# Kernel optimization log

Measured on AMD Instinct MI355X. Metric: run time of the kernel, lower is better.

## Reference

```python
import jax, jax.numpy as jnp
import numpy as np

ALPHA = 0.2   # LeakyReLU negative slope (init arg alpha)
H = 256       # hidden_dim
U = 1024      # user pairs -> 2U user nodes
M = 64        # UAV nodes
D = 2 * U     # uniform out-degree per UAV (edges sorted by source)
N = 2 * U + M
E = M * D


def _lstm_dir(x, w_ih, w_hh, b):
    # x: [T, B, I] -> outputs [T, B, Hc]; b = b_ih + b_hh (they only ever add)
    Hc = w_hh.shape[1]
    B = x.shape[1]
    def step(carry, xt):
        h, c = carry
        g = xt @ w_ih.T + h @ w_hh.T + b          # [B, 4*Hc], gate order i,f,g,o
        i, f, gg, o = jnp.split(g, 4, axis=-1)
        c = jax.nn.sigmoid(f) * c + jax.nn.sigmoid(i) * jnp.tanh(gg)
        h = jax.nn.sigmoid(o) * jnp.tanh(c)
        return (h, c), h
    h0 = jnp.zeros((B, Hc), x.dtype)
    _, hs = jax.lax.scan(step, (h0, h0), x)
    return hs


def _bilstm(x, wih, whh, b):
    # wih: [2, 4Hc, I]; whh: [2, 4Hc, Hc]; b: [2, 4Hc]; dir 0 = fwd, 1 = reverse
    fwd = _lstm_dir(x, wih[0], whh[0], b[0])
    rev = _lstm_dir(x[::-1], wih[1], whh[1], b[1])[::-1]
    return jnp.concatenate([fwd, rev], axis=-1)   # [T, B, 2*Hc]


def _mlp2(h, w1, b1, w2, b2):
    h = jax.nn.relu(h @ w1.T + b1)
    return jax.nn.relu(h @ w2.T + b2)


def _forward(x, edge_index, users_num,
             ul_wih, ul_whh, ul_b, uav_lin_w, uav_lin_b,
             msg_w1, msg_b1, msg_w2, msg_b2,
             wq_w, wq_b, wr_w, wr_b, att_w, att_b,
             upd_w1, upd_b1, upd_w2, upd_b2,
             uavl_wih, uavl_whh, uavl_b, lin2_w, lin2_b):
    Un = users_num
    n = x.shape[0]
    m = n - 2 * Un
    # ---- users bidirectional LSTM over the pair (seq_len=2, batch=U) ----
    seq = jnp.stack([x[:Un], x[Un:2 * Un]], axis=0)        # [2, U, 2]
    users = _bilstm(seq, ul_wih, ul_whh, ul_b)             # [2, U, H]
    users = jnp.concatenate([users[0], users[1]], axis=0)  # [2U, H]
    uavs = x[2 * Un:] @ uav_lin_w.T + uav_lin_b            # [M, H]
    h = jnp.concatenate([users, uavs], axis=0)             # [N, H]
    # ---- message passing (flow target_to_source: i=src, aggregate at src) ----
    src, tgt = edge_index[0], edge_index[1]
    xi = h[src]                                            # [E, H]
    xj = h[tgt]                                            # [E, H]
    msg = _mlp2(jnp.concatenate([xi, xj], axis=1), msg_w1, msg_b1, msg_w2, msg_b2)  # [E, H]
    q = xi @ wq_w.T + wq_b
    r = msg @ wr_w.T + wr_b
    a = jax.nn.leaky_relu(jnp.concatenate([q, r], axis=1) @ att_w.T + att_b, ALPHA)  # [E,1]
    # segment softmax: edges sorted by source, uniform degree -> reshape [M, D]
    a = jax.nn.softmax(a.reshape(m, -1), axis=1).reshape(-1, 1)
    # ---- scatter-mean aggregate over source index ----
    agg = jax.ops.segment_sum(a * msg, src, num_segments=n)          # [N, H]
    cnt = jax.ops.segment_sum(jnp.ones((src.shape[0],), x.dtype), src, num_segments=n)
    agg = agg / jnp.maximum(cnt, 1.0)[:, None]
    # ---- update ----
    h2 = _mlp2(jnp.concatenate([agg, h], axis=1), upd_w1, upd_b1, upd_w2, upd_b2)  # [N, H]
    uav_seq = h2[2 * Un:][:, None, :]                      # [M, 1, H]
    uav_out = _bilstm(uav_seq, uavl_wih, uavl_whh, uavl_b)[:, 0, :]  # [M, H]
    out = jnp.concatenate([h2[:2 * Un], uav_out], axis=0)
    return jax.nn.sigmoid(out @ lin2_w.T + lin2_b)         # [N, 2]


def setup_inputs():
    key = jax.random.key(0)
    ks = iter(jax.random.split(key, 32))
    p = lambda *s: jax.random.normal(next(ks), s, jnp.float32) * 0.05
    Hc = H // 2
    x = jax.random.uniform(next(ks), (N, 2), jnp.float32)
    src = jnp.repeat(2 * U + jnp.arange(M), D)
    tgt = jnp.tile(jnp.arange(2 * U), M)
    edge_index = jnp.stack([src, tgt]).astype(jnp.int32)
    return dict(
        x=x, edge_index=edge_index, users_num=U,
        ul_wih=p(2, 4 * Hc, 2), ul_whh=p(2, 4 * Hc, Hc), ul_b=p(2, 4 * Hc),
        uav_lin_w=p(H, 2), uav_lin_b=p(H),
        msg_w1=p(H, 2 * H), msg_b1=p(H), msg_w2=p(H, H), msg_b2=p(H),
        wq_w=p(H, H), wq_b=p(H), wr_w=p(H, H), wr_b=p(H),
        att_w=p(1, 2 * H), att_b=p(1),
        upd_w1=p(H, 2 * H), upd_b1=p(H), upd_w2=p(H, H), upd_b2=p(H),
        uavl_wih=p(2, 4 * Hc, H), uavl_whh=p(2, 4 * Hc, Hc), uavl_b=p(2, 4 * Hc),
        lin2_w=p(2, H), lin2_b=p(2),
    )


def reference(x, edge_index, users_num,
              ul_wih, ul_whh, ul_b, uav_lin_w, uav_lin_b,
              msg_w1, msg_b1, msg_w2, msg_b2,
              wq_w, wq_b, wr_w, wr_b, att_w, att_b,
              upd_w1, upd_b1, upd_w2, upd_b2,
              uavl_wih, uavl_whh, uavl_b, lin2_w, lin2_b):
    return _forward(x, edge_index, users_num,
                    ul_wih, ul_whh, ul_b, uav_lin_w, uav_lin_b,
                    msg_w1, msg_b1, msg_w2, msg_b2,
                    wq_w, wq_b, wr_w, wr_b, att_w, att_b,
                    upd_w1, upd_b1, upd_w2, upd_b2,
                    uavl_wih, uavl_whh, uavl_b, lin2_w, lin2_b)
```

## Files before the change

kernel.cpp:

```cpp
#include <hip/hip_runtime.h>
#include <hip/hip_bf16.h>
#include <math.h>

#define UQ   1024
#define NUQ  2048
#define MQ   64
#define NN   2112
#define HD   256

typedef __attribute__((ext_vector_type(4))) float f32x4;
typedef __attribute__((ext_vector_type(8))) __bf16 bf16x8;

#define OFF_HB    0u
#define OFF_HUF   65536u
#define OFF_PUBF  1146880u
#define OFF_PB    2195456u
#define OFF_SPR   2260992u
#define OFF_ATT   2261248u
#define OFF_WHHT  2263552u
#define OFF_WIHT  2787840u
#define OFF_W1F   3836416u
#define OFF_W2F   4098560u
#define OFF_UW1F  4229632u
#define OFF_UW2F  4491776u
#define OFF_CREC  4622848u
#define OFF_H2U   5155328u
#define OFF_PART  5220864u

__device__ __forceinline__ float sigm(float v) { return 1.f / (1.f + expf(-v)); }

__device__ __forceinline__ int huf_idx(int row, int k) {
  return (((row >> 6) * 8 + (k >> 5)) * 4 + ((row >> 4) & 3)) * 512 +
         (((k >> 3) & 3) * 16 + (row & 15)) * 8 + (k & 7);
}
__device__ __forceinline__ int pubf_idx(int row, int k) {
  return (((row >> 8) * 8 + (k >> 5)) * 16 + ((row >> 4) & 15)) * 512 +
         (((k >> 3) & 3) * 16 + (row & 15)) * 8 + (k & 7);
}

__device__ __forceinline__ void gl16(const void* g, void* l) {
  __builtin_amdgcn_global_load_lds((const __attribute__((address_space(1))) void*)g,
                                   (__attribute__((address_space(3))) void*)l, 16, 0, 0);
}

__device__ void tile_transpose_perm(const float* __restrict__ in, int in_ld,
                                    float* __restrict__ out, int out_ld,
                                    int k0, int c0) {
  __shared__ float ldt[64][68];
  const int t = threadIdx.x;
  {
    const int ci = t >> 2, kq = t & 3;
    const int c = c0 + ci;
    const int row = (c & 3) * 128 + (c >> 2);
    const float* src = in + row * in_ld + k0 + kq * 16;
#pragma unroll
    for (int e = 0; e < 4; ++e)
      *(f32x4*)&ldt[ci][kq * 16 + e * 4] = *(const f32x4*)(src + e * 4);
  }
  __syncthreads();
  {
    const int kk = t >> 2, cq = t & 3;
    float* dst = out + (k0 + kk) * out_ld + c0 + cq * 16;
#pragma unroll
    for (int e4 = 0; e4 < 4; ++e4) {
      f32x4 v;
#pragma unroll
      for (int j = 0; j < 4; ++j) v[j] = ldt[cq * 16 + e4 * 4 + j][kk];
      *(f32x4*)(dst + e4 * 4) = v;
    }
  }
}

template<int K>
__device__ void frag_cast16(const float* __restrict__ W, int j0, __bf16* __restrict__ frag) {
  __shared__ float ldc[16][K + 4];
  const int t = threadIdx.x;
  {
    const int jr = t >> 4, kq = t & 15;
    const float* src = W + (j0 + jr) * K + kq * (K / 16);
#pragma unroll
    for (int e = 0; e < K / 64; ++e)
      *(f32x4*)&ldc[jr][kq * (K / 16) + e * 4] = *(const f32x4*)(src + e * 4);
  }
  __syncthreads();
  const int f = j0 >> 4;
  constexpr int nks = K >> 5;
  constexpr int thr_per_ks = 256 / nks;
  constexpr int q_per_thr = 512 / thr_per_ks;
  const int ks = t / thr_per_ks;
  const int q0 = (t % thr_per_ks) * q_per_thr;
#pragma unroll
  for (int h = 0; h < q_per_thr / 8; ++h) {
    bf16x8 v;
#pragma unroll
    for (int e = 0; e < 8; ++e) {
      int q = q0 + h * 8 + e;
      int lane = q >> 3;
      v[e] = (__bf16)ldc[lane & 15][ks * 32 + (lane >> 4) * 8 + (q & 7)];
    }
    *(bf16x8*)(frag + (ks * 16 + f) * 512 + q0 + h * 8) = v;
  }
}

__global__ __launch_bounds__(256) void k0_prep(
    const float* __restrict__ ul_whh, const float* __restrict__ uavl_wih,
    const float* __restrict__ msg_w1, const float* __restrict__ msg_w2,
    const float* __restrict__ upd_w1, const float* __restrict__ upd_w2,
    const float* __restrict__ att_w,  const float* __restrict__ att_b,
    const float* __restrict__ wq_w,   const float* __restrict__ wq_b,
    const float* __restrict__ wr_w,   const float* __restrict__ wr_b,
    char* __restrict__ ws)
{
  const int b = blockIdx.x, t = threadIdx.x;
  if (b < 32) {
    const int dir = b >> 4, tile = b & 15;
    tile_transpose_perm(ul_whh + dir * 65536, 128,
                        (float*)(ws + OFF_WHHT) + dir * 65536, 512,
                        (tile >> 3) * 64, (tile & 7) * 64);
  } else if (b < 96) {
    const int b2 = b - 32, dir = b2 >> 5, tile = b2 & 31;
    tile_transpose_perm(uavl_wih + dir * 131072, 256,
                        (float*)(ws + OFF_WIHT) + dir * 131072, 512,
                        (tile >> 3) * 64, (tile & 7) * 64);
  } else if (b < 112) {
    frag_cast16<256>(msg_w2, (b - 96) * 16, (__bf16*)(ws + OFF_W2F));
  } else if (b < 128) {
    frag_cast16<512>(msg_w1, (b - 112) * 16, (__bf16*)(ws + OFF_W1F));
  } else if (b < 144) {
    frag_cast16<512>(upd_w1, (b - 128) * 16, (__bf16*)(ws + OFF_UW1F));
  } else if (b < 160) {
    frag_cast16<256>(upd_w2, (b - 144) * 16, (__bf16*)(ws + OFF_UW2F));
  } else {
    float* wqa = (float*)(ws + OFF_ATT);
    float* vv  = wqa + 256;
    float* c0  = wqa + 512;
    float sa = 0.f, sr = 0.f;
    for (int j = 0; j < 256; ++j) {
      sa += att_w[j]       * wq_w[j * 256 + t];
      sr += att_w[256 + j] * wr_w[j * 256 + t];
    }
    wqa[t] = sa; vv[t] = sr;
    __shared__ float red[256];
    red[t] = att_w[t] * wq_b[t] + att_w[256 + t] * wr_b[t];
    __syncthreads();
    for (int s = 128; s > 0; s >>= 1) { if (t < s) red[t] += red[t + s]; __syncthreads(); }
    if (t == 0) c0[0] = red[0] + att_b[0];
  }
}

__global__ __launch_bounds__(256) void k1_embed(
    const float* __restrict__ x, const float* __restrict__ ul_wih,
    const float* __restrict__ ul_b, const float* __restrict__ uav_lin_w,
    const float* __restrict__ uav_lin_b, char* __restrict__ ws)
{
  __bf16* huf = (__bf16*)(ws + OFF_HUF);
  const int b = blockIdx.x, tid = threadIdx.x;
  if (b < 256) {
    const float* whhT = (const float*)(ws + OFF_WHHT);
    const int dir = tid >> 7, hc = tid & 127;
    const int u0 = b * 4;
    float wx[4], wy[4], bb[4];
#pragma unroll
    for (int g = 0; g < 4; ++g) {
      int row = g * 128 + hc;
      wx[g] = ul_wih[dir * 1024 + row * 2 + 0];
      wy[g] = ul_wih[dir * 1024 + row * 2 + 1];
      bb[g] = ul_b[dir * 512 + row];
    }
    __shared__ float h1s[2][128][4];
    __shared__ float hout[8][260];
    float c1[4], h1v[4], in1x[4], in1y[4];
#pragma unroll
    for (int uu = 0; uu < 4; ++uu) {
      int u = u0 + uu;
      float ax = x[u * 2], ay = x[u * 2 + 1];
      float bx = x[(UQ + u) * 2], by = x[(UQ + u) * 2 + 1];
      float i0x = dir ? bx : ax, i0y = dir ? by : ay;
      in1x[uu] = dir ? ax : bx; in1y[uu] = dir ? ay : by;
      float gv[4];
#pragma unroll
      for (int g = 0; g < 4; ++g) gv[g] = wx[g] * i0x + wy[g] * i0y + bb[g];
      float ii = sigm(gv[0]), gg = tanhf(gv[2]), oo = sigm(gv[3]);
      c1[uu] = ii * gg;
      h1v[uu] = oo * tanhf(c1[uu]);
      h1s[dir][hc][uu] = h1v[uu];
    }
    __syncthreads();
    float acc[4][4];
#pragma unroll
    for (int uu = 0; uu < 4; ++uu)
#pragma unroll
      for (int g = 0; g < 4; ++g) acc[uu][g] = wx[g] * in1x[uu] + wy[g] * in1y[uu] + bb[g];
    for (int k = 0; k < 128; ++k) {
      f32x4 hv  = *(const f32x4*)&h1s[dir][k][0];
      f32x4 wv4 = *(const f32x4*)(whhT + dir * 65536 + k * 512 + hc * 4);
#pragma unroll
      for (int uu = 0; uu < 4; ++uu)
#pragma unroll
        for (int g = 0; g < 4; ++g) acc[uu][g] += hv[uu] * wv4[g];
    }
    const int col = dir * 128 + hc;
#pragma unroll
    for (int uu = 0; uu < 4; ++uu) {
      float ii = sigm(acc[uu][0]), ff = sigm(acc[uu][1]);
      float gg = tanhf(acc[uu][2]), oo = sigm(acc[uu][3]);
      float c2 = ff * c1[uu] + ii * gg;
      float h2v = oo * tanhf(c2);
      float va = dir ? h2v : h1v[uu];
      float vb = dir ? h1v[uu] : h2v;
      hout[uu][col] = va;
      hout[4 + uu][col] = vb;
    }
    __syncthreads();
    {
      const int lr = tid >> 5, c = tid & 31;
      bf16x8 v;
#pragma unroll
      for (int e = 0; e < 8; ++e) v[e] = (__bf16)hout[lr][c * 8 + e];
      const int node = (lr < 4) ? (u0 + lr) : (UQ + u0 + lr - 4);
      *(bf16x8*)(huf + huf_idx(node, c * 8)) = v;
    }
  } else {
    float* hb = (float*)(ws + OFF_HB);
    const int j = tid;
    const int mb = (b - 256) * 16;
    for (int m = mb; m < mb + 16; ++m) {
      float xa = x[(NUQ + m) * 2], xb = x[(NUQ + m) * 2 + 1];
      float val = xa * uav_lin_w[j * 2] + xb * uav_lin_w[j * 2 + 1] + uav_lin_b[j];
      hb[m * 256 + j] = val;
      huf[huf_idx(NUQ + m, j)] = (__bf16)val;
    }
  }
}

template<int G, int NKS>
__device__ __forceinline__ void frag_gemm_acc_g(const __bf16* __restrict__ Abase, int g0,
                                                const __bf16* __restrict__ Bbase,
                                                f32x4 acc[G][4]) {
  const int lane = threadIdx.x & 63;
  const int cg = threadIdx.x >> 6;
  for (int ks = 0; ks < NKS; ++ks) {
    bf16x8 Af[G], Bf[4];
#pragma unroll
    for (int g = 0; g < G; ++g)
      Af[g] = *(const bf16x8*)(Abase + ((ks * 4 + g0 + g) * 64 + lane) * 8);
#pragma unroll
    for (int f = 0; f < 4; ++f)
      Bf[f] = *(const bf16x8*)(Bbase + ((ks * 16 + cg * 4 + f) * 64 + lane) * 8);
#pragma unroll
    for (int g = 0; g < G; ++g)
#pragma unroll
      for (int f = 0; f < 4; ++f)
        acc[g][f] = __builtin_amdgcn_mfma_f32_16x16x32_bf16(Af[g], Bf[f], acc[g][f], 0, 0, 0);
  }
}

__global__ __launch_bounds__(256) void k2_proj(const float* __restrict__ msg_b1,
                                               char* __restrict__ ws)
{
  const __bf16* huf = (const __bf16*)(ws + OFF_HUF);
  const __bf16* w1f = (const __bf16*)(ws + OFF_W1F);
  const int b = blockIdx.x;
  const int lane = threadIdx.x & 63, cg = threadIdx.x >> 6;
  const int cl = lane & 15, g16 = lane >> 4;
  if (b < 64) {
    f32x4 acc[2][4] = {};
    frag_gemm_acc_g<2, 8>(huf + (b >> 1) * 16384, (b & 1) * 2, w1f + 65536, acc);
    __bf16* pubf = (__bf16*)(ws + OFF_PUBF);
#pragma unroll
    for (int g = 0; g < 2; ++g)
#pragma unroll
      for (int f = 0; f < 4; ++f)
#pragma unroll
        for (int r = 0; r < 4; ++r) {
          int row = b * 32 + g * 16 + g16 * 4 + r;
          int col = cg * 64 + f * 16 + cl;
          pubf[pubf_idx(row, col)] = (__bf16)acc[g][f][r];
        }
  } else if (b == 64) {
    f32x4 acc[4][4] = {};
    frag_gemm_acc_g<4, 8>(huf + 32 * 16384, 0, w1f, acc);
    float* pb = (float*)(ws + OFF_PB);
#pragma unroll
    for (int g = 0; g < 4; ++g)
#pragma unroll
      for (int f = 0; f < 4; ++f)
#pragma unroll
        for (int r = 0; r < 4; ++r) {
          int row = g * 16 + g16 * 4 + r;
          int col = cg * 64 + f * 16 + cl;
          pb[row * 256 + col] = acc[g][f][r] + msg_b1[col];
        }
  } else {
    const float* hb  = (const float*)(ws + OFF_HB);
    const float* wqa = (const float*)(ws + OFF_ATT);
    const float* c0  = wqa + 512;
    float* spr = (float*)(ws + OFF_SPR);
    const int t = threadIdx.x;
    if (t < 64) {
      float s = 0.f;
      for (int k = 0; k < 256; ++k) s += hb[t * 256 + k] * wqa[k];
      spr[t] = s + c0[0];
    }
  }
}

__global__ __launch_bounds__(1024, 2) void k3_edge(const float* __restrict__ msg_b2,
                                                   char* __restrict__ ws)
{
  const char*  PUBF = (const char*)(ws + OFF_PUBF);
  const float* PB   = (const float*)(ws + OFF_PB);
  const float* spr  = (const float*)(ws + OFF_SPR);
  const float* vv   = (const float*)(ws + OFF_ATT) + 256;
  const char*  W2F  = (const char*)(ws + OFF_W2F);
  float* crec = (float*)(ws + OFF_CREC);

  __shared__ __align__(16) char bufA[2][16384];
  __shared__ __align__(16) char bufB[2][16384];
  __shared__ float plds[16][64];
  __shared__ float redmax[16], wds[16];
  __shared__ float wvs[4][256];

  const int m = blockIdx.x >> 3, ch = blockIdx.x & 7;
  const int tid = threadIdx.x, wave = tid >> 6, lane = tid & 63;
  const int cl = lane & 15, g16 = lane >> 4;
  const int rg = wave >> 2, cg = wave & 3;
  const int rot = (m + ch) & 7;
  const float sm = spr[m];
  const char* Asrc = PUBF + ch * 131072;
  const float* pbm = PB + m * 256;

  {
    bf16x8 araw = *(const bf16x8*)(Asrc + rot * 16384 + wave * 1024 + lane * 16);
    gl16(W2F + rot * 16384 + wave * 1024 + lane * 16, &bufB[0][wave * 1024]);
    const float* pbp = pbm + rot * 32 + (lane >> 4) * 8;
    f32x4 p0 = *(const f32x4*)pbp, p1 = *(const f32x4*)(pbp + 4);
    bf16x8 a;
#pragma unroll
    for (int r = 0; r < 4; ++r) {
      a[r]     = (__bf16)fmaxf((float)araw[r]     + p0[r], 0.f);
      a[4 + r] = (__bf16)fmaxf((float)araw[4 + r] + p1[r], 0.f);
    }
    *(bf16x8*)(&bufA[0][wave * 1024 + lane * 16]) = a;
  }
  __syncthreads();

  f32x4 acc[4][4] = {};
  for (int i = 0; i < 8; ++i) {
    const int cur = i & 1;
    bf16x8 arn{};
    f32x4 pn0{}, pn1{};
    if (i < 7) {
      const int ksn = (i + 1 + rot) & 7;
      arn = *(const bf16x8*)(Asrc + ksn * 16384 + wave * 1024 + lane * 16);
      gl16(W2F + ksn * 16384 + wave * 1024 + lane * 16, &bufB[cur ^ 1][wave * 1024]);
      const float* pbp = pbm + ksn * 32 + (lane >> 4) * 8;
      pn0 = *(const f32x4*)pbp;
      pn1 = *(const f32x4*)(pbp + 4);
    }
    bf16x8 Af[4], Bf[4];
#pragma unroll
    for (int g = 0; g < 4; ++g)
      Af[g] = *(const bf16x8*)(&bufA[cur][((rg * 4 + g) * 64 + lane) * 16]);
#pragma unroll
    for (int f = 0; f < 4; ++f)
      Bf[f] = *(const bf16x8*)(&bufB[cur][((cg * 4 + f) * 64 + lane) * 16]);
    __builtin_amdgcn_s_setprio(1);
#pragma unroll
    for (int g = 0; g < 4; ++g)
#pragma unroll
      for (int f = 0; f < 4; ++f)
        acc[g][f] = __builtin_amdgcn_mfma_f32_16x16x32_bf16(Af[g], Bf[f], acc[g][f], 0, 0, 0);
    __builtin_amdgcn_s_setprio(0);
    if (i < 7) {
      bf16x8 a;
#pragma unroll
      for (int r = 0; r < 4; ++r) {
        a[r]     = (__bf16)fmaxf((float)arn[r]     + pn0[r], 0.f);
        a[4 + r] = (__bf16)fmaxf((float)arn[4 + r] + pn1[r], 0.f);
      }
      *(bf16x8*)(&bufA[cur ^ 1][wave * 1024 + lane * 16]) = a;
    }
    __syncthreads();
  }

  float p[4][4] = {};
#pragma unroll
  for (int f = 0; f < 4; ++f) {
    const int j = cg * 64 + f * 16 + cl;
    const float b2j = msg_b2[j], vj = vv[j];
#pragma unroll
    for (int g = 0; g < 4; ++g)
#pragma unroll
      for (int r = 0; r < 4; ++r) {
        float mv = fmaxf(acc[g][f][r] + b2j, 0.f);
        acc[g][f][r] = mv;
        p[g][r] += mv * vj;
      }
  }
#pragma unroll
  for (int mask = 1; mask < 16; mask <<= 1)
#pragma unroll
    for (int g = 0; g < 4; ++g)
#pragma unroll
      for (int r = 0; r < 4; ++r) p[g][r] += __shfl_xor(p[g][r], mask);
  if (cl == 0) {
#pragma unroll
    for (int g = 0; g < 4; ++g)
#pragma unroll
      for (int r = 0; r < 4; ++r) plds[wave][g * 16 + g16 * 4 + r] = p[g][r];
  }
  __syncthreads();

  float lr[4][4], wm = -3.4e38f;
#pragma unroll
  for (int g = 0; g < 4; ++g)
#pragma unroll
    for (int r = 0; r < 4; ++r) {
      int row = g * 16 + g16 * 4 + r;
      float l = plds[rg * 4 + 0][row] + plds[rg * 4 + 1][row] +
                plds[rg * 4 + 2][row] + plds[rg * 4 + 3][row] + sm;
      l = l > 0.f ? l : 0.2f * l;
      lr[g][r] = l;
      wm = fmaxf(wm, l);
    }
  wm = fmaxf(wm, __shfl_xor(wm, 16));
  wm = fmaxf(wm, __shfl_xor(wm, 32));
  if (lane == 0) redmax[wave] = wm;
  __syncthreads();
  float Mc = redmax[0];
#pragma unroll
  for (int i = 1; i < 16; ++i) Mc = fmaxf(Mc, redmax[i]);

  float e[4][4], ds = 0.f;
#pragma unroll
  for (int g = 0; g < 4; ++g)
#pragma unroll
    for (int r = 0; r < 4; ++r) { e[g][r] = __expf(lr[g][r] - Mc); ds += e[g][r]; }
  ds += __shfl_xor(ds, 16);
  ds += __shfl_xor(ds, 32);
  if (lane == 0) wds[wave] = ds;

#pragma unroll
  for (int f = 0; f < 4; ++f) {
    float w = 0.f;
#pragma unroll
    for (int g = 0; g < 4; ++g)
#pragma unroll
      for (int r = 0; r < 4; ++r) w += e[g][r] * acc[g][f][r];
    w += __shfl_xor(w, 16);
    w += __shfl_xor(w, 32);
    if (g16 == 0) wvs[rg][cg * 64 + f * 16 + cl] = w;
  }
  __syncthreads();

  float* rec = crec + (m * 8 + ch) * 260;
  if (tid < 256) rec[tid] = wvs[0][tid] + wvs[1][tid] + wvs[2][tid] + wvs[3][tid];
  if (tid == 0) rec[256] = Mc;
  if (tid == 1) rec[257] = wds[0] + wds[4] + wds[8] + wds[12];
}

__global__ __launch_bounds__(256) void k56_update(
    const float* __restrict__ upd_b1, const float* __restrict__ upd_b2,
    const float* __restrict__ lin2_w, const float* __restrict__ lin2_b,
    float* __restrict__ out, char* __restrict__ ws)
{
  const __bf16* huf  = (const __bf16*)(ws + OFF_HUF);
  const __bf16* uw1f = (const __bf16*)(ws + OFF_UW1F);
  const __bf16* uw2f = (const __bf16*)(ws + OFF_UW2F);

  __shared__ __align__(16) __bf16 l1f[8 * 2 * 512];
  __shared__ __align__(16) __bf16 aggf[8 * 2 * 512];
  __shared__ float scs[32][8];
  __shared__ float sS[32];
  __shared__ float l2p[4][32][2];

  const int b = blockIdx.x, tid = threadIdx.x;
  const int lane = tid & 63, cg = tid >> 6;
  const int cl = lane & 15, g16 = lane >> 4;

  f32x4 acc[2][4] = {};
  if (b < 64) {
    frag_gemm_acc_g<2, 8>(huf + (b >> 1) * 16384, (b & 1) * 2, uw1f + 8 * 16 * 512, acc);
  } else {
    const int m0 = (b - 64) * 32;
    const float* crec = (const float*)(ws + OFF_CREC);
    if (tid < 32) {
      const int m = m0 + tid;
      float mx = -3.4e38f;
      for (int c = 0; c < 8; ++c) mx = fmaxf(mx, crec[(m * 8 + c) * 260 + 256]);
      float S = 0.f;
      for (int c = 0; c < 8; ++c) {
        float sc = __expf(crec[(m * 8 + c) * 260 + 256] - mx);
        scs[tid][c] = sc;
        S += sc * crec[(m * 8 + c) * 260 + 257];
      }
      sS[tid] = S;
    }
    __syncthreads();
    for (int ml = 0; ml < 32; ++ml) {
      float A = 0.f;
#pragma unroll
      for (int c = 0; c < 8; ++c) A += scs[ml][c] * crec[((m0 + ml) * 8 + c) * 260 + tid];
      float agg = A / sS[ml] * (1.f / 2048.f);
      aggf[((tid >> 5) * 2 + (ml >> 4)) * 512 + (((tid >> 3) & 3) * 16 + (ml & 15)) * 8 + (tid & 7)] =
          (__bf16)agg;
    }
    __syncthreads();
    const int g0 = (b - 64) * 2;
    const __bf16* hufu = huf + 32 * 16384;
    for (int ks = 0; ks < 8; ++ks) {
      bf16x8 Af[2], Bf[4];
#pragma unroll
      for (int g = 0; g < 2; ++g)
        Af[g] = *(const bf16x8*)(aggf + ((ks * 2 + g) * 64 + lane) * 8);
#pragma unroll
      for (int f = 0; f < 4; ++f)
        Bf[f] = *(const bf16x8*)(uw1f + ((ks * 16 + cg * 4 + f) * 64 + lane) * 8);
#pragma unroll
      for (int g = 0; g < 2; ++g)
#pragma unroll
        for (int f = 0; f < 4; ++f)
          acc[g][f] = __builtin_amdgcn_mfma_f32_16x16x32_bf16(Af[g], Bf[f], acc[g][f], 0, 0, 0);
    }
    for (int ks = 8; ks < 16; ++ks) {
      bf16x8 Af[2], Bf[4];
#pragma unroll
      for (int g = 0; g < 2; ++g)
        Af[g] = *(const bf16x8*)(hufu + (((ks - 8) * 4 + g0 + g) * 64 + lane) * 8);
#pragma unroll
      for (int f = 0; f < 4; ++f)
        Bf[f] = *(const bf16x8*)(uw1f + ((ks * 16 + cg * 4 + f) * 64 + lane) * 8);
#pragma unroll
      for (int g = 0; g < 2; ++g)
#pragma unroll
        for (int f = 0; f < 4; ++f)
          acc[g][f] = __builtin_amdgcn_mfma_f32_16x16x32_bf16(Af[g], Bf[f], acc[g][f], 0, 0, 0);
    }
  }

#pragma unroll
  for (int g = 0; g < 2; ++g)
#pragma unroll
    for (int f = 0; f < 4; ++f) {
      const int col = cg * 64 + f * 16 + cl;
      const float b1 = upd_b1[col];
#pragma unroll
      for (int r = 0; r < 4; ++r) {
        float v = fmaxf(acc[g][f][r] + b1, 0.f);
        l1f[((col >> 5) * 2 + g) * 512 + (((col >> 3) & 3) * 16 + g16 * 4 + r) * 8 + (col & 7)] =
            (__bf16)v;
      }
    }
  __syncthreads();

  f32x4 a2[2][4] = {};
  for (int ks = 0; ks < 8; ++ks) {
    bf16x8 Af[2], Bf[4];
#pragma unroll
    for (int g = 0; g < 2; ++g)
      Af[g] = *(const bf16x8*)(l1f + ((ks * 2 + g) * 64 + lane) * 8);
#pragma unroll
    for (int f = 0; f < 4; ++f)
      Bf[f] = *(const bf16x8*)(uw2f + ((ks * 16 + cg * 4 + f) * 64 + lane) * 8);
#pragma unroll
    for (int g = 0; g < 2; ++g)
#pragma unroll
      for (int f = 0; f < 4; ++f)
        a2[g][f] = __builtin_amdgcn_mfma_f32_16x16x32_bf16(Af[g], Bf[f], a2[g][f], 0, 0, 0);
  }

  if (b < 64) {
    float d0[2][4] = {}, d1[2][4] = {};
#pragma unroll
    for (int f = 0; f < 4; ++f) {
      const int col = cg * 64 + f * 16 + cl;
      const float b2 = upd_b2[col];
      const float w0 = lin2_w[col], w1 = lin2_w[256 + col];
#pragma unroll
      for (int g = 0; g < 2; ++g)
#pragma unroll
        for (int r = 0; r < 4; ++r) {
          float hv = fmaxf(a2[g][f][r] + b2, 0.f);
          d0[g][r] += hv * w0;
          d1[g][r] += hv * w1;
        }
    }
#pragma unroll
    for (int mask = 1; mask < 16; mask <<= 1)
#pragma unroll
      for (int g = 0; g < 2; ++g)
#pragma unroll
        for (int r = 0; r < 4; ++r) {
          d0[g][r] += __shfl_xor(d0[g][r], mask);
          d1[g][r] += __shfl_xor(d1[g][r], mask);
        }
    if (cl == 0) {
#pragma unroll
      for (int g = 0; g < 2; ++g)
#pragma unroll
        for (int r = 0; r < 4; ++r) {
          l2p[cg][g * 16 + g16 * 4 + r][0] = d0[g][r];
          l2p[cg][g * 16 + g16 * 4 + r][1] = d1[g][r];
        }
    }
    __syncthreads();
    if (tid < 32) {
      float s0 = l2p[0][tid][0] + l2p[1][tid][0] + l2p[2][tid][0] + l2p[3][tid][0] + lin2_b[0];
      float s1 = l2p[0][tid][1] + l2p[1][tid][1] + l2p[2][tid][1] + l2p[3][tid][1] + lin2_b[1];
      const int row = b * 32 + tid;
      out[row * 2 + 0] = 1.f / (1.f + expf(-s0));
      out[row * 2 + 1] = 1.f / (1.f + expf(-s1));
    }
  } else {
    float* h2u = (float*)(ws + OFF_H2U);
    const int m0 = (b - 64) * 32;
#pragma unroll
    for (int g = 0; g < 2; ++g)
#pragma unroll
      for (int f = 0; f < 4; ++f) {
        const int col = cg * 64 + f * 16 + cl;
        const float b2 = upd_b2[col];
#pragma unroll
        for (int r = 0; r < 4; ++r) {
          const int rl = g * 16 + g16 * 4 + r;
          h2u[(m0 + rl) * 256 + col] = fmaxf(a2[g][f][r] + b2, 0.f);
        }
      }
  }
}

__global__ __launch_bounds__(256) void k7a_gates(char* __restrict__ ws)
{
  const float* h2u  = (const float*)(ws + OFF_H2U);
  const float* wihT = (const float*)(ws + OFF_WIHT);
  float* part = (float*)(ws + OFF_PART);
  const int m = blockIdx.x >> 2, kq = blockIdx.x & 3;
  const int tid = threadIdx.x;
  const int dir = tid >> 7, hc = tid & 127;
  __shared__ float xs[64];
  if (tid < 64) xs[tid] = h2u[m * 256 + kq * 64 + tid];
  __syncthreads();
  f32x4 a4 = {0.f, 0.f, 0.f, 0.f};
  for (int k = 0; k < 64; ++k) {
    float xv = xs[k];
    f32x4 wv4 = *(const f32x4*)(wihT + dir * 131072 + (kq * 64 + k) * 512 + hc * 4);
#pragma unroll
    for (int g = 0; g < 4; ++g) a4[g] += xv * wv4[g];
  }
  *(f32x4*)(part + (m * 4 + kq) * 1024 + dir * 512 + hc * 4) = a4;
}

__global__ __launch_bounds__(256) void k7b_final(
    const float* __restrict__ uavl_b, const float* __restrict__ lin2_w,
    const float* __restrict__ lin2_b, float* __restrict__ out, char* __restrict__ ws)
{
  const float* part = (const float*)(ws + OFF_PART);
  const int m = blockIdx.x, tid = threadIdx.x;
  const int dir = tid >> 7, hc = tid & 127;
  f32x4 a4 = {0.f, 0.f, 0.f, 0.f};
#pragma unroll
  for (int kq = 0; kq < 4; ++kq) {
    f32x4 p = *(const f32x4*)(part + (m * 4 + kq) * 1024 + dir * 512 + hc * 4);
#pragma unroll
    for (int g = 0; g < 4; ++g) a4[g] += p[g];
  }
  float bb[4];
#pragma unroll
  for (int g = 0; g < 4; ++g) bb[g] = uavl_b[dir * 512 + g * 128 + hc];
  __shared__ float uo[256];
  float ii = sigm(a4[0] + bb[0]);
  float gg = tanhf(a4[2] + bb[2]);
  float oo = sigm(a4[3] + bb[3]);
  float cc = ii * gg;
  uo[dir * 128 + hc] = oo * tanhf(cc);
  __syncthreads();
  float p0 = uo[tid] * lin2_w[tid];
  float p1 = uo[tid] * lin2_w[256 + tid];
#pragma unroll
  for (int mask = 1; mask < 64; mask <<= 1) {
    p0 += __shfl_xor(p0, mask);
    p1 += __shfl_xor(p1, mask);
  }
  __shared__ float r0s[4], r1s[4];
  const int lane = tid & 63, wv = tid >> 6;
  if (lane == 0) { r0s[wv] = p0; r1s[wv] = p1; }
  __syncthreads();
  if (tid == 0) {
    float d0 = r0s[0] + r0s[1] + r0s[2] + r0s[3] + lin2_b[0];
    float d1 = r1s[0] + r1s[1] + r1s[2] + r1s[3] + lin2_b[1];
    out[(NUQ + m) * 2 + 0] = 1.f / (1.f + expf(-d0));
    out[(NUQ + m) * 2 + 1] = 1.f / (1.f + expf(-d1));
  }
}

extern "C" void kernel_launch(void* const* d_in, const int* in_sizes, int n_in,
                              void* d_out, int out_size, void* d_ws, size_t ws_size,
                              hipStream_t stream)
{
  const float* x         = (const float*)d_in[0];
  const float* ul_wih    = (const float*)d_in[3];
  const float* ul_whh    = (const float*)d_in[4];
  const float* ul_b      = (const float*)d_in[5];
  const float* uav_lin_w = (const float*)d_in[6];
  const float* uav_lin_b = (const float*)d_in[7];
  const float* msg_w1    = (const float*)d_in[8];
  const float* msg_b1    = (const float*)d_in[9];
  const float* msg_w2    = (const float*)d_in[10];
  const float* msg_b2    = (const float*)d_in[11];
  const float* wq_w      = (const float*)d_in[12];
  const float* wq_b      = (const float*)d_in[13];
  const float* wr_w      = (const float*)d_in[14];
  const float* wr_b      = (const float*)d_in[15];
  const float* att_w     = (const float*)d_in[16];
  const float* att_b     = (const float*)d_in[17];
  const float* upd_w1    = (const float*)d_in[18];
  const float* upd_b1    = (const float*)d_in[19];
  const float* upd_w2    = (const float*)d_in[20];
  const float* upd_b2    = (const float*)d_in[21];
  const float* uavl_wih  = (const float*)d_in[22];
  const float* uavl_b    = (const float*)d_in[24];
  const float* lin2_w    = (const float*)d_in[25];
  const float* lin2_b    = (const float*)d_in[26];
  char* ws = (char*)d_ws;
  float* out = (float*)d_out;

  k0_prep<<<dim3(161), dim3(256), 0, stream>>>(ul_whh, uavl_wih, msg_w1, msg_w2, upd_w1,
                                               upd_w2, att_w, att_b, wq_w, wq_b, wr_w, wr_b, ws);
  k1_embed<<<dim3(260), dim3(256), 0, stream>>>(x, ul_wih, ul_b, uav_lin_w, uav_lin_b, ws);
  k2_proj<<<dim3(66), dim3(256), 0, stream>>>(msg_b1, ws);
  k3_edge<<<dim3(512), dim3(1024), 0, stream>>>(msg_b2, ws);
  k56_update<<<dim3(66), dim3(256), 0, stream>>>(upd_b1, upd_b2, lin2_w, lin2_b, out, ws);
  k7a_gates<<<dim3(256), dim3(256), 0, stream>>>(ws);
  k7b_final<<<dim3(64), dim3(256), 0, stream>>>(uavl_b, lin2_w, lin2_b, out, ws);
}
```

Before: 94.51 us.

## Move user update MLP into edge kernel and coalesce projection stores via LDS

The user-node update MLP and the final lin2/sigmoid output, previously computed by 64 blocks of k56_update, now run as 64 extra blocks appended to the k3_edge launch. This lets them overlap with edge processing, and k56_update shrinks to the two UAV blocks. k2_proj now stages its accumulator tile in shared memory and writes the fragment-layout bf16 buffer with 16-byte vector stores instead of scattered scalar stores. An unroll pragma is added to the LSTM recurrence loop. The extra blocks use only 256 of 1024 threads, which may idle waves and occupy CUs the edge blocks need.

```diff
diff --git a/kernel.cpp b/kernel.cpp
--- a/kernel.cpp
+++ b/kernel.cpp
@@ -191,6 +191,7 @@
     for (int uu = 0; uu < 4; ++uu)
 #pragma unroll
       for (int g = 0; g < 4; ++g) acc[uu][g] = wx[g] * in1x[uu] + wy[g] * in1y[uu] + bb[g];
+#pragma unroll 4
     for (int k = 0; k < 128; ++k) {
       f32x4 hv  = *(const f32x4*)&h1s[dir][k][0];
       f32x4 wv4 = *(const f32x4*)(whhT + dir * 65536 + k * 512 + hc * 4);
@@ -238,7 +239,7 @@
                                                 const __bf16* __restrict__ Bbase,
                                                 f32x4 acc[G][4]) {
   const int lane = threadIdx.x & 63;
-  const int cg = threadIdx.x >> 6;
+  const int cg = (threadIdx.x >> 6) & 3;
   for (int ks = 0; ks < NKS; ++ks) {
     bf16x8 Af[G], Bf[4];
 #pragma unroll
@@ -261,22 +262,35 @@
   const __bf16* huf = (const __bf16*)(ws + OFF_HUF);
   const __bf16* w1f = (const __bf16*)(ws + OFF_W1F);
   const int b = blockIdx.x;
-  const int lane = threadIdx.x & 63, cg = threadIdx.x >> 6;
+  const int tid = threadIdx.x;
+  const int lane = tid & 63, cg = tid >> 6;
   const int cl = lane & 15, g16 = lane >> 4;
   if (b < 64) {
     f32x4 acc[2][4] = {};
     frag_gemm_acc_g<2, 8>(huf + (b >> 1) * 16384, (b & 1) * 2, w1f + 65536, acc);
+    __shared__ float ldt[32][264];
+#pragma unroll
+    for (int g = 0; g < 2; ++g)
+#pragma unroll
+      for (int f = 0; f < 4; ++f)
+#pragma unroll
+        for (int r = 0; r < 4; ++r)
+          ldt[g * 16 + g16 * 4 + r][cg * 64 + f * 16 + cl] = acc[g][f][r];
+    __syncthreads();
     __bf16* pubf = (__bf16*)(ws + OFF_PUBF);
-#pragma unroll
-    for (int g = 0; g < 2; ++g)
-#pragma unroll
-      for (int f = 0; f < 4; ++f)
-#pragma unroll
-        for (int r = 0; r < 4; ++r) {
-          int row = b * 32 + g * 16 + g16 * 4 + r;
-          int col = cg * 64 + f * 16 + cl;
-          pubf[pubf_idx(row, col)] = (__bf16)acc[g][f][r];
-        }
+    const int c2 = b >> 3, r16base = (b & 7) * 2;
+#pragma unroll
+    for (int p = 0; p < 4; ++p) {
+      const int region = p * 4 + (tid >> 6);
+      const int ks = region >> 1, r16l = region & 1;
+      const int row15 = tid & 15, kg = (tid >> 4) & 3;
+      const int row = r16l * 16 + row15;
+      bf16x8 v;
+#pragma unroll
+      for (int j = 0; j < 8; ++j) v[j] = (__bf16)ldt[row][ks * 32 + kg * 8 + j];
+      const int dst = ((c2 * 8 + ks) * 16 + (r16base + r16l)) * 512 + (kg * 16 + row15) * 8;
+      *(bf16x8*)(pubf + dst) = v;
+    }
   } else if (b == 64) {
     f32x4 acc[4][4] = {};
     frag_gemm_acc_g<4, 8>(huf + 32 * 16384, 0, w1f, acc);
@@ -296,18 +310,120 @@
     const float* wqa = (const float*)(ws + OFF_ATT);
     const float* c0  = wqa + 512;
     float* spr = (float*)(ws + OFF_SPR);
-    const int t = threadIdx.x;
-    if (t < 64) {
+    if (tid < 64) {
       float s = 0.f;
-      for (int k = 0; k < 256; ++k) s += hb[t * 256 + k] * wqa[k];
-      spr[t] = s + c0[0];
-    }
-  }
-}
-
-__global__ __launch_bounds__(1024, 2) void k3_edge(const float* __restrict__ msg_b2,
-                                                   char* __restrict__ ws)
+      for (int k = 0; k < 256; ++k) s += hb[tid * 256 + k] * wqa[k];
+      spr[tid] = s + c0[0];
+    }
+  }
+}
+
+__global__ __launch_bounds__(1024, 2) void k3_edge(
+    const float* __restrict__ msg_b2,
+    const float* __restrict__ upd_b1, const float* __restrict__ upd_b2,
+    const float* __restrict__ lin2_w, const float* __restrict__ lin2_b,
+    float* __restrict__ out, char* __restrict__ ws)
 {
+  __shared__ __align__(16) char bufA[2][16384];
+  __shared__ __align__(16) char bufB[2][16384];
+  __shared__ float plds[16][64];
+  __shared__ float redmax[16], wds[16];
+  __shared__ float wvs[4][256];
+
+  const int tid = threadIdx.x, wave = tid >> 6, lane = tid & 63;
+  const int cl = lane & 15, g16 = lane >> 4;
+
+  if (blockIdx.x >= 512) {
+    const int b = blockIdx.x - 512;
+    const __bf16* huf  = (const __bf16*)(ws + OFF_HUF);
+    const __bf16* uw1f = (const __bf16*)(ws + OFF_UW1F);
+    const __bf16* uw2f = (const __bf16*)(ws + OFF_UW2F);
+    __bf16* l1f = (__bf16*)&bufA[0][0];
+    float*  l2p = (float*)&bufB[0][0];
+    const int cg4 = (tid >> 6) & 3;
+
+    f32x4 acc[2][4] = {};
+    if (tid < 256) {
+      frag_gemm_acc_g<2, 8>(huf + (b >> 1) * 16384, (b & 1) * 2, uw1f + 8 * 16 * 512, acc);
+#pragma unroll
+      for (int g = 0; g < 2; ++g)
+#pragma unroll
+        for (int f = 0; f < 4; ++f) {
+          const int col = cg4 * 64 + f * 16 + cl;
+          const float b1 = upd_b1[col];
+#pragma unroll
+          for (int r = 0; r < 4; ++r) {
+            float v = fmaxf(acc[g][f][r] + b1, 0.f);
+            l1f[((col >> 5) * 2 + g) * 512 + (((col >> 3) & 3) * 16 + g16 * 4 + r) * 8 + (col & 7)] =
+                (__bf16)v;
+          }
+        }
+    }
+    __syncthreads();
+
+    if (tid < 256) {
+      f32x4 a2[2][4] = {};
+      for (int ks = 0; ks < 8; ++ks) {
+        bf16x8 Af[2], Bf[4];
+#pragma unroll
+        for (int g = 0; g < 2; ++g)
+          Af[g] = *(const bf16x8*)(l1f + ((ks * 2 + g) * 64 + lane) * 8);
+#pragma unroll
+        for (int f = 0; f < 4; ++f)
+          Bf[f] = *(const bf16x8*)(uw2f + ((ks * 16 + cg4 * 4 + f) * 64 + lane) * 8);
+#pragma unroll
+        for (int g = 0; g < 2; ++g)
+#pragma unroll
+          for (int f = 0; f < 4; ++f)
+            a2[g][f] = __builtin_amdgcn_mfma_f32_16x16x32_bf16(Af[g], Bf[f], a2[g][f], 0, 0, 0);
+      }
+      float d0[2][4] = {}, d1[2][4] = {};
+#pragma unroll
+      for (int f = 0; f < 4; ++f) {
+        const int col = cg4 * 64 + f * 16 + cl;
+        const float b2 = upd_b2[col];
+        const float w0 = lin2_w[col], w1 = lin2_w[256 + col];
+#pragma unroll
+        for (int g = 0; g < 2; ++g)
+#pragma unroll
+          for (int r = 0; r < 4; ++r) {
+            float hv = fmaxf(a2[g][f][r] + b2, 0.f);
+            d0[g][r] += hv * w0;
+            d1[g][r] += hv * w1;
+          }
+      }
+#pragma unroll
+      for (int mask = 1; mask < 16; mask <<= 1)
+#pragma unroll
+        for (int g = 0; g < 2; ++g)
+#pragma unroll
+          for (int r = 0; r < 4; ++r) {
+            d0[g][r] += __shfl_xor(d0[g][r], mask);
+            d1[g][r] += __shfl_xor(d1[g][r], mask);
+          }
+      if (cl == 0) {
+#pragma unroll
+        for (int g = 0; g < 2; ++g)
+#pragma unroll
+          for (int r = 0; r < 4; ++r) {
+            l2p[(cg4 * 32 + g * 16 + g16 * 4 + r) * 2 + 0] = d0[g][r];
+            l2p[(cg4 * 32 + g * 16 + g16 * 4 + r) * 2 + 1] = d1[g][r];
+          }
+      }
+    }
+    __syncthreads();
+    if (tid < 32) {
+      float s0 = l2p[(0 * 32 + tid) * 2 + 0] + l2p[(1 * 32 + tid) * 2 + 0] +
+                 l2p[(2 * 32 + tid) * 2 + 0] + l2p[(3 * 32 + tid) * 2 + 0] + lin2_b[0];
+      float s1 = l2p[(0 * 32 + tid) * 2 + 1] + l2p[(1 * 32 + tid) * 2 + 1] +
+                 l2p[(2 * 32 + tid) * 2 + 1] + l2p[(3 * 32 + tid) * 2 + 1] + lin2_b[1];
+      const int row = b * 32 + tid;
+      out[row * 2 + 0] = 1.f / (1.f + expf(-s0));
+      out[row * 2 + 1] = 1.f / (1.f + expf(-s1));
+    }
+    return;
+  }
+
   const char*  PUBF = (const char*)(ws + OFF_PUBF);
   const float* PB   = (const float*)(ws + OFF_PB);
   const float* spr  = (const float*)(ws + OFF_SPR);
@@ -315,15 +431,7 @@
   const char*  W2F  = (const char*)(ws + OFF_W2F);
   float* crec = (float*)(ws + OFF_CREC);
 
-  __shared__ __align__(16) char bufA[2][16384];
-  __shared__ __align__(16) char bufB[2][16384];
-  __shared__ float plds[16][64];
-  __shared__ float redmax[16], wds[16];
-  __shared__ float wvs[4][256];
-
   const int m = blockIdx.x >> 3, ch = blockIdx.x & 7;
-  const int tid = threadIdx.x, wave = tid >> 6, lane = tid & 63;
-  const int cl = lane & 15, g16 = lane >> 4;
   const int rg = wave >> 2, cg = wave & 3;
   const int rot = (m + ch) & 7;
   const float sm = spr[m];
@@ -331,9 +439,9 @@
   const float* pbm = PB + m * 256;
 
   {
-    bf16x8 araw = *(const bf16x8*)(Asrc + rot * 16384 + wave * 1024 + lane * 16);
-    gl16(W2F + rot * 16384 + wave * 1024 + lane * 16, &bufB[0][wave * 1024]);
-    const float* pbp = pbm + rot * 32 + (lane >> 4) * 8;
+    bf16x8 araw = *(const bf16x8*)(Asrc + rot * 16384 + tid * 16);
+    gl16(W2F + rot * 16384 + tid * 16, &bufB[0][tid * 16]);
+    const float* pbp = pbm + rot * 32 + (tid >> 4 & 3) * 8;
     f32x4 p0 = *(const f32x4*)pbp, p1 = *(const f32x4*)(pbp + 4);
     bf16x8 a;
 #pragma unroll
@@ -341,7 +449,7 @@
       a[r]     = (__bf16)fmaxf((float)araw[r]     + p0[r], 0.f);
       a[4 + r] = (__bf16)fmaxf((float)araw[4 + r] + p1[r], 0.f);
     }
-    *(bf16x8*)(&bufA[0][wave * 1024 + lane * 16]) = a;
+    *(bf16x8*)(&bufA[0][tid * 16]) = a;
   }
   __syncthreads();
 
@@ -352,9 +460,9 @@
     f32x4 pn0{}, pn1{};
     if (i < 7) {
       const int ksn = (i + 1 + rot) & 7;
-      arn = *(const bf16x8*)(Asrc + ksn * 16384 + wave * 1024 + lane * 16);
-      gl16(W2F + ksn * 16384 + wave * 1024 + lane * 16, &bufB[cur ^ 1][wave * 1024]);
-      const float* pbp = pbm + ksn * 32 + (lane >> 4) * 8;
+      arn = *(const bf16x8*)(Asrc + ksn * 16384 + tid * 16);
+      gl16(W2F + ksn * 16384 + tid * 16, &bufB[cur ^ 1][tid * 16]);
+      const float* pbp = pbm + ksn * 32 + (tid >> 4 & 3) * 8;
       pn0 = *(const f32x4*)pbp;
       pn1 = *(const f32x4*)(pbp + 4);
     }
@@ -379,7 +487,7 @@
         a[r]     = (__bf16)fmaxf((float)arn[r]     + pn0[r], 0.f);
         a[4 + r] = (__bf16)fmaxf((float)arn[4 + r] + pn1[r], 0.f);
       }
-      *(bf16x8*)(&bufA[cur ^ 1][wave * 1024 + lane * 16]) = a;
+      *(bf16x8*)(&bufA[cur ^ 1][tid * 16]) = a;
     }
     __syncthreads();
   }
@@ -462,8 +570,7 @@
 
 __global__ __launch_bounds__(256) void k56_update(
     const float* __restrict__ upd_b1, const float* __restrict__ upd_b2,
-    const float* __restrict__ lin2_w, const float* __restrict__ lin2_b,
-    float* __restrict__ out, char* __restrict__ ws)
+    char* __restrict__ ws)
 {
   const __bf16* huf  = (const __bf16*)(ws + OFF_HUF);
   const __bf16* uw1f = (const __bf16*)(ws + OFF_UW1F);
@@ -473,70 +580,66 @@
   __shared__ __align__(16) __bf16 aggf[8 * 2 * 512];
   __shared__ float scs[32][8];
   __shared__ float sS[32];
-  __shared__ float l2p[4][32][2];
 
   const int b = blockIdx.x, tid = threadIdx.x;
   const int lane = tid & 63, cg = tid >> 6;
   const int cl = lane & 15, g16 = lane >> 4;
 
+  const int m0 = b * 32;
+  const float* crec = (const float*)(ws + OFF_CREC);
+  if (tid < 32) {
+    const int m = m0 + tid;
+    float mx = -3.4e38f;
+    for (int c = 0; c < 8; ++c) mx = fmaxf(mx, crec[(m * 8 + c) * 260 + 256]);
+    float S = 0.f;
+    for (int c = 0; c < 8; ++c) {
+      float sc = __expf(crec[(m * 8 + c) * 260 + 256] - mx);
+      scs[tid][c] = sc;
+      S += sc * crec[(m * 8 + c) * 260 + 257];
+    }
+    sS[tid] = S;
+  }
+  __syncthreads();
+  for (int ml = 0; ml < 32; ++ml) {
+    float A = 0.f;
+#pragma unroll
+    for (int c = 0; c < 8; ++c) A += scs[ml][c] * crec[((m0 + ml) * 8 + c) * 260 + tid];
+    float agg = A / sS[ml] * (1.f / 2048.f);
+    aggf[((tid >> 5) * 2 + (ml >> 4)) * 512 + (((tid >> 3) & 3) * 16 + (ml & 15)) * 8 + (tid & 7)] =
+        (__bf16)agg;
+  }
+  __syncthreads();
+
   f32x4 acc[2][4] = {};
-  if (b < 64) {
-    frag_gemm_acc_g<2, 8>(huf + (b >> 1) * 16384, (b & 1) * 2, uw1f + 8 * 16 * 512, acc);
-  } else {
-    const int m0 = (b - 64) * 32;
-    const float* crec = (const float*)(ws + OFF_CREC);
-    if (tid < 32) {
-      const int m = m0 + tid;
-      float mx = -3.4e38f;
-      for (int c = 0; c < 8; ++c) mx = fmaxf(mx, crec[(m * 8 + c) * 260 + 256]);
-      float S = 0.f;
-      for (int c = 0; c < 8; ++c) {
-        float sc = __expf(crec[(m * 8 + c) * 260 + 256] - mx);
-        scs[tid][c] = sc;
-        S += sc * crec[(m * 8 + c) * 260 + 257];
-      }
-      sS[tid] = S;
-    }
-    __syncthreads();
-    for (int ml = 0; ml < 32; ++ml) {
-      float A = 0.f;
-#pragma unroll
-      for (int c = 0; c < 8; ++c) A += scs[ml][c] * crec[((m0 + ml) * 8 + c) * 260 + tid];
-      float agg = A / sS[ml] * (1.f / 2048.f);
-      aggf[((tid >> 5) * 2 + (ml >> 4)) * 512 + (((tid >> 3) & 3) * 16 + (ml & 15)) * 8 + (tid & 7)] =
-          (__bf16)agg;
-    }
-    __syncthreads();
-    const int g0 = (b - 64) * 2;
-    const __bf16* hufu = huf + 32 * 16384;
-    for (int ks = 0; ks < 8; ++ks) {
-      bf16x8 Af[2], Bf[4];
-#pragma unroll
-      for (int g = 0; g < 2; ++g)
-        Af[g] = *(const bf16x8*)(aggf + ((ks * 2 + g) * 64 + lane) * 8);
+  const int g0 = b * 2;
+  const __bf16* hufu = huf + 32 * 16384;
+  for (int ks = 0; ks < 8; ++ks) {
+    bf16x8 Af[2], Bf[4];
+#pragma unroll
+    for (int g = 0; g < 2; ++g)
+      Af[g] = *(const bf16x8*)(aggf + ((ks * 2 + g) * 64 + lane) * 8);
+#pragma unroll
+    for (int f = 0; f < 4; ++f)
+      Bf[f] = *(const bf16x8*)(uw1f + ((ks * 16 + cg * 4 + f) * 64 + lane) * 8);
+#pragma unroll
+    for (int g = 0; g < 2; ++g)
 #pragma unroll
       for (int f = 0; f < 4; ++f)
-        Bf[f] = *(const bf16x8*)(uw1f + ((ks * 16 + cg * 4 + f) * 64 + lane) * 8);
-#pragma unroll
-      for (int g = 0; g < 2; ++g)
-#pragma unroll
-        for (int f = 0; f < 4; ++f)
-          acc[g][f] = __builtin_amdgcn_mfma_f32_16x16x32_bf16(Af[g], Bf[f], acc[g][f], 0, 0, 0);
-    }
-    for (int ks = 8; ks < 16; ++ks) {
-      bf16x8 Af[2], Bf[4];
-#pragma unroll
-      for (int g = 0; g < 2; ++g)
-        Af[g] = *(const bf16x8*)(hufu + (((ks - 8) * 4 + g0 + g) * 64 + lane) * 8);
+        acc[g][f] = __builtin_amdgcn_mfma_f32_16x16x32_bf16(Af[g], Bf[f], acc[g][f], 0, 0, 0);
+  }
+  for (int ks = 8; ks < 16; ++ks) {
+    bf16x8 Af[2], Bf[4];
+#pragma unroll
+    for (int g = 0; g < 2; ++g)
+      Af[g] = *(const bf16x8*)(hufu + (((ks - 8) * 4 + g0 + g) * 64 + lane) * 8);
+#pragma unroll
+    for (int f = 0; f < 4; ++f)
+      Bf[f] = *(const bf16x8*)(uw1f + ((ks * 16 + cg * 4 + f) * 64 + lane) * 8);
+#pragma unroll
+    for (int g = 0; g < 2; ++g)
 #pragma unroll
       for (int f = 0; f < 4; ++f)
-        Bf[f] = *(const bf16x8*)(uw1f + ((ks * 16 + cg * 4 + f) * 64 + lane) * 8);
-#pragma unroll
-      for (int g = 0; g < 2; ++g)
-#pragma unroll
-        for (int f = 0; f < 4; ++f)
-          acc[g][f] = __builtin_amdgcn_mfma_f32_16x16x32_bf16(Af[g], Bf[f], acc[g][f], 0, 0, 0);
-    }
+        acc[g][f] = __builtin_amdgcn_mfma_f32_16x16x32_bf16(Af[g], Bf[f], acc[g][f], 0, 0, 0);
   }
 
 #pragma unroll
@@ -570,64 +673,19 @@
         a2[g][f] = __builtin_amdgcn_mfma_f32_16x16x32_bf16(Af[g], Bf[f], a2[g][f], 0, 0, 0);
   }
 
-  if (b < 64) {
-    float d0[2][4] = {}, d1[2][4] = {};
+  float* h2u = (float*)(ws + OFF_H2U);
+#pragma unroll
+  for (int g = 0; g < 2; ++g)
 #pragma unroll
     for (int f = 0; f < 4; ++f) {
       const int col = cg * 64 + f * 16 + cl;
       const float b2 = upd_b2[col];
-      const float w0 = lin2_w[col], w1 = lin2_w[256 + col];
-#pragma unroll
-      for (int g = 0; g < 2; ++g)
-#pragma unroll
-        for (int r = 0; r < 4; ++r) {
-          float hv = fmaxf(a2[g][f][r] + b2, 0.f);
-          d0[g][r] += hv * w0;
-          d1[g][r] += hv * w1;
-        }
-    }
-#pragma unroll
-    for (int mask = 1; mask < 16; mask <<= 1)
-#pragma unroll
-      for (int g = 0; g < 2; ++g)
-#pragma unroll
-        for (int r = 0; r < 4; ++r) {
-          d0[g][r] += __shfl_xor(d0[g][r], mask);
-          d1[g][r] += __shfl_xor(d1[g][r], mask);
-        }
-    if (cl == 0) {
-#pragma unroll
-      for (int g = 0; g < 2; ++g)
-#pragma unroll
-        for (int r = 0; r < 4; ++r) {
-          l2p[cg][g * 16 + g16 * 4 + r][0] = d0[g][r];
-          l2p[cg][g * 16 + g16 * 4 + r][1] = d1[g][r];
-        }
-    }
-    __syncthreads();
-    if (tid < 32) {
-      float s0 = l2p[0][tid][0] + l2p[1][tid][0] + l2p[2][tid][0] + l2p[3][tid][0] + lin2_b[0];
-      float s1 = l2p[0][tid][1] + l2p[1][tid][1] + l2p[2][tid][1] + l2p[3][tid][1] + lin2_b[1];
-      const int row = b * 32 + tid;
-      out[row * 2 + 0] = 1.f / (1.f + expf(-s0));
-      out[row * 2 + 1] = 1.f / (1.f + expf(-s1));
-    }
-  } else {
-    float* h2u = (float*)(ws + OFF_H2U);
-    const int m0 = (b - 64) * 32;
-#pragma unroll
-    for (int g = 0; g < 2; ++g)
-#pragma unroll
-      for (int f = 0; f < 4; ++f) {
-        const int col = cg * 64 + f * 16 + cl;
-        const float b2 = upd_b2[col];
-#pragma unroll
-        for (int r = 0; r < 4; ++r) {
-          const int rl = g * 16 + g16 * 4 + r;
-          h2u[(m0 + rl) * 256 + col] = fmaxf(a2[g][f][r] + b2, 0.f);
-        }
+#pragma unroll
+      for (int r = 0; r < 4; ++r) {
+        const int rl = g * 16 + g16 * 4 + r;
+        h2u[(m0 + rl) * 256 + col] = fmaxf(a2[g][f][r] + b2, 0.f);
       }
-  }
+    }
 }
 
 __global__ __launch_bounds__(256) void k7a_gates(char* __restrict__ ws)
@@ -729,8 +787,8 @@
                                                upd_w2, att_w, att_b, wq_w, wq_b, wr_w, wr_b, ws);
   k1_embed<<<dim3(260), dim3(256), 0, stream>>>(x, ul_wih, ul_b, uav_lin_w, uav_lin_b, ws);
   k2_proj<<<dim3(66), dim3(256), 0, stream>>>(msg_b1, ws);
-  k3_edge<<<dim3(512), dim3(1024), 0, stream>>>(msg_b2, ws);
-  k56_update<<<dim3(66), dim3(256), 0, stream>>>(upd_b1, upd_b2, lin2_w, lin2_b, out, ws);
+  k3_edge<<<dim3(576), dim3(1024), 0, stream>>>(msg_b2, upd_b1, upd_b2, lin2_w, lin2_b, out, ws);
+  k56_update<<<dim3(2), dim3(256), 0, stream>>>(upd_b1, upd_b2, ws);
   k7a_gates<<<dim3(256), dim3(256), 0, stream>>>(ws);
   k7b_final<<<dim3(64), dim3(256), 0, stream>>>(uavl_b, lin2_w, lin2_b, out, ws);
 }
```

Result: slower. 101.0 us (+6.9%).
